# Optimization experiments

Hardware: AMD Instinct MI355X
Metric: run time of the kernel (lower is better)

Reference implementation:

```python
import jax, jax.numpy as jnp
import numpy as np

B, L, D = 4096, 50, 64
NU, NI, NR = 100000, 100000, 5


def setup_inputs() -> dict:
    key = jax.random.key(0)
    ks = jax.random.split(key, 16)
    s = 0.02
    inp = {
        "nodes_v": jax.random.randint(ks[0], (B,), 0, NI),
        "neigh_u": jax.random.randint(ks[1], (B, L), 0, NU),
        "neigh_r": jax.random.randint(ks[2], (B, L), 0, NR),
        "embed_u": jax.random.normal(ks[3], (NU, D)) * s,
        "embed_i": jax.random.normal(ks[4], (NI, D)) * s,
        "embed_r": jax.random.normal(ks[5], (NR, D)) * s,
        # gv MLP: Linear(2D,D) ReLU Linear(D,D) ReLU Linear(D,D)
        "gv_w1": jax.random.normal(ks[6], (2 * D, D)) * s, "gv_b1": jnp.zeros((D,)),
        "gv_w2": jax.random.normal(ks[7], (D, D)) * s,     "gv_b2": jnp.zeros((D,)),
        "gv_w3": jax.random.normal(ks[8], (D, D)) * s,     "gv_b3": jnp.zeros((D,)),
        # attention MLP: Linear(2D,D) ReLU Linear(D,D) ReLU Linear(D,1), softmax over neighbors
        "att_w1": jax.random.normal(ks[9], (2 * D, D)) * s, "att_b1": jnp.zeros((D,)),
        "att_w2": jax.random.normal(ks[10], (D, D)) * s,    "att_b2": jnp.zeros((D,)),
        "att_w3": jax.random.normal(ks[11], (D, 1)) * s,    "att_b3": jnp.zeros((1,)),
        # combine: Linear(2D,D) ReLU Linear(D,D) ReLU
        "wr1_w": jax.random.normal(ks[12], (2 * D, D)) * s, "wr1_b": jnp.zeros((D,)),
        "wr2_w": jax.random.normal(ks[13], (D, D)) * s,     "wr2_b": jnp.zeros((D,)),
    }
    return inp


def reference(nodes_v, neigh_u, neigh_r, embed_u, embed_i, embed_r,
              gv_w1, gv_b1, gv_w2, gv_b2, gv_w3, gv_b3,
              att_w1, att_b1, att_w2, att_b2, att_w3, att_b3,
              wr1_w, wr1_b, wr2_w, wr2_b):
    qj = embed_i[nodes_v]            # [B, D] item reps
    pt = embed_u[neigh_u]            # [B, L, D] neighbor user reps
    er = embed_r[neigh_r]            # [B, L, D] rating reps
    # fusion MLP g(.)
    x = jnp.concatenate([pt, er], axis=-1)                    # [B, L, 2D]
    h = jax.nn.relu(x @ gv_w1 + gv_b1)
    h = jax.nn.relu(h @ gv_w2 + gv_b2)
    fjt = h @ gv_w3 + gv_b3                                   # [B, L, D]
    # attention over neighbors (dropout is identity in eval mode)
    q_rep = jnp.broadcast_to(qj[:, None, :], fjt.shape)       # [B, L, D]
    a = jnp.concatenate([fjt, q_rep], axis=-1)                # [B, L, 2D]
    a = jax.nn.relu(a @ att_w1 + att_b1)
    a = jax.nn.relu(a @ att_w2 + att_b2)
    scores = (a @ att_w3 + att_b3)[..., 0]                    # [B, L]
    mu = jax.nn.softmax(scores, axis=1)                       # softmax over neighbors
    zj = jnp.einsum("bld,bl->bd", fjt, mu)                   # weighted aggregation
    # combine aggregated neighborhood with item's own embedding (2D -> D)
    z = jax.nn.relu(jnp.concatenate([zj, qj], axis=-1) @ wr1_w + wr1_b)
    out = jax.nn.relu(z @ wr2_w + wr2_b)                      # [B, D]
    return out
```

## Files before the change

kernel.cpp:

```cpp
#include <hip/hip_runtime.h>

typedef __bf16 bf16;
typedef short s16x8 __attribute__((ext_vector_type(8)));
typedef __bf16 b16x8 __attribute__((ext_vector_type(8)));
typedef float f32x4 __attribute__((ext_vector_type(4)));

#define B_   4096
#define L_   50
#define SH   72

#define OFF_W1F  0
#define OFF_W2F  8192
#define OFF_W3F  12288
#define OFF_WCF  16384
#define OFF_A2F  20480
#define OFF_R1T  24576
#define OFF_R2T  32768
#define WT_TOTAL 36864
#define BIAS1P_BYTE 73728
#define CQ_BYTE     73984
#define EU16_BYTE   1122560
#define ER16_BYTE   13922560
#define WS_NEED     13923200

#define PREP_W_BLOCKS 145
#define PREP_C_BLOCKS 1024
#define CONV_THREADS  800040
#define CONV_BLOCKS   3126

__device__ __forceinline__ unsigned short f2b(float f) {
    __bf16 h = (__bf16)f;
    return __builtin_bit_cast(unsigned short, h);
}
__device__ __forceinline__ unsigned pack2(float a, float b) {
    return (unsigned)f2b(a) | ((unsigned)f2b(b) << 16);
}
__device__ __forceinline__ s16x8 mkfrag(float4 a, float4 b) {
    union { s16x8 v; unsigned u[4]; } r;
    r.u[0] = pack2(a.x, a.y); r.u[1] = pack2(a.z, a.w);
    r.u[2] = pack2(b.x, b.y); r.u[3] = pack2(b.z, b.w);
    return r.v;
}
__device__ __forceinline__ f32x4 mfma16(s16x8 a, s16x8 b, f32x4 c) {
    return __builtin_amdgcn_mfma_f32_16x16x32_bf16(a, b, c, 0, 0, 0);
}

extern "C" __global__ void prep_all(const float* __restrict__ w1, const float* __restrict__ w2,
                                    const float* __restrict__ w3, const float* __restrict__ a1,
                                    const float* __restrict__ a2, const float* __restrict__ r1,
                                    const float* __restrict__ r2, const float* __restrict__ gb3,
                                    const float* __restrict__ ab1,
                                    const int* __restrict__ nodes_v, const float* __restrict__ embed_i,
                                    const float* __restrict__ embed_u, const float* __restrict__ embed_r,
                                    bf16* __restrict__ wt, float* __restrict__ bias1p,
                                    float* __restrict__ cq,
                                    bf16* __restrict__ eu16, bf16* __restrict__ er16)
{
    if (blockIdx.x >= PREP_W_BLOCKS + PREP_C_BLOCKS) {
        long t = (long)(blockIdx.x - PREP_W_BLOCKS - PREP_C_BLOCKS) * 256 + threadIdx.x;
        if (t < 800000) {
            const float* s = embed_u + t * 8;
            float4 a = *(const float4*)s, b = *(const float4*)(s + 4);
            *(s16x8*)(eu16 + t * 8) = mkfrag(a, b);
        } else if (t < CONV_THREADS) {
            long r = (t - 800000) * 8;
            const float* s = embed_r + r;
            float4 a = *(const float4*)s, b = *(const float4*)(s + 4);
            *(s16x8*)(er16 + r) = mkfrag(a, b);
        }
        return;
    }
    if (blockIdx.x >= PREP_W_BLOCKS) {
        int gid = (blockIdx.x - PREP_W_BLOCKS) * 256 + threadIdx.x;
        int b = gid >> 6, n = gid & 63;
        int v = nodes_v[b];
        const float* q = embed_i + v * 64;
        float s0 = 0.f, s1 = 0.f, s2 = 0.f, s3 = 0.f;
#pragma unroll
        for (int k = 0; k < 64; k += 4) {
            s0 = fmaf(q[k],     a1[(64 + k) * 64 + n],     s0);
            s1 = fmaf(q[k + 1], a1[(64 + k + 1) * 64 + n], s1);
            s2 = fmaf(q[k + 2], a1[(64 + k + 2) * 64 + n], s2);
            s3 = fmaf(q[k + 3], a1[(64 + k + 3) * 64 + n], s3);
        }
        cq[gid] = (s0 + s1) + (s2 + s3);
        return;
    }
    int i = blockIdx.x * 256 + threadIdx.x;
    if (i >= WT_TOTAL + 64) return;
    if (i >= WT_TOTAL) {
        int n = i - WT_TOTAL;
        float s0 = ab1[n], s1 = 0.f, s2 = 0.f, s3 = 0.f;
#pragma unroll
        for (int t = 0; t < 64; t += 4) {
            s0 = fmaf(gb3[t],     a1[t * 64 + n],       s0);
            s1 = fmaf(gb3[t + 1], a1[(t + 1) * 64 + n], s1);
            s2 = fmaf(gb3[t + 2], a1[(t + 2) * 64 + n], s2);
            s3 = fmaf(gb3[t + 3], a1[(t + 3) * 64 + n], s3);
        }
        bias1p[n] = (s0 + s1) + (s2 + s3);
        return;
    }
    float val;
    if (i < OFF_R1T) {
        int off, kind;
        if      (i < OFF_W2F) { off = OFF_W1F; kind = 0; }
        else if (i < OFF_W3F) { off = OFF_W2F; kind = 1; }
        else if (i < OFF_WCF) { off = OFF_W3F; kind = 2; }
        else if (i < OFF_A2F) { off = OFF_WCF; kind = 3; }
        else                  { off = OFF_A2F; kind = 4; }
        int local = i - off;
        int f = local >> 9, lane = (local >> 3) & 63, j = local & 7;
        int kt = f >> 2, nt = f & 3, quad = lane >> 4, m = lane & 15;
        int k = kt * 32 + quad * 8 + j;
        int n = nt * 16 + m;
        if (kind == 0)      val = w1[k * 64 + n];
        else if (kind == 1) val = w2[k * 64 + n];
        else if (kind == 2) val = w3[k * 64 + n];
        else if (kind == 4) val = a2[k * 64 + n];
        else {
            float s0 = 0.f, s1 = 0.f, s2 = 0.f, s3 = 0.f;
#pragma unroll
            for (int t = 0; t < 64; t += 4) {
                float4 w = *(const float4*)(w3 + k * 64 + t);
                s0 = fmaf(w.x, a1[t * 64 + n],       s0);
                s1 = fmaf(w.y, a1[(t + 1) * 64 + n], s1);
                s2 = fmaf(w.z, a1[(t + 2) * 64 + n], s2);
                s3 = fmaf(w.w, a1[(t + 3) * 64 + n], s3);
            }
            val = (s0 + s1) + (s2 + s3);
        }
    }
    else if (i < OFF_R2T) { int li = i - OFF_R1T; int n = li >> 7, k = li & 127; val = r1[k * 64 + n]; }
    else                  { int li = i - OFF_R2T; int n = li >> 6, k = li & 63;  val = r2[k * 64 + n]; }
    wt[i] = (bf16)val;
}

template<bool BF16E>
__global__ void __launch_bounds__(128, 4)
dense_fused(const int* __restrict__ nodes_v, const int* __restrict__ neigh_u,
            const int* __restrict__ neigh_r,
            const float* __restrict__ embed_u, const float* __restrict__ embed_i,
            const float* __restrict__ embed_r,
            const float* __restrict__ gv_b1, const float* __restrict__ gv_b2,
            const float* __restrict__ gv_b3,
            const float* __restrict__ att_b2, const float* __restrict__ att_w3,
            const float* __restrict__ wr1_b, const float* __restrict__ wr2_b,
            const bf16* __restrict__ wt, const bf16* __restrict__ eu16,
            const bf16* __restrict__ er16, const float* __restrict__ cq,
            const float* __restrict__ bias1p, float* __restrict__ out)
{
    __shared__ __align__(16) bf16 H[64 * SH];
    __shared__ float zp[2 * 64];
    __shared__ float swm[2 * 2];
    __shared__ float qsh[64];

    const int tid = threadIdx.x;
    const int lane = tid & 63, wave = tid >> 6;
    const int m = lane & 15, quad = lane >> 4;
    const int b = blockIdx.x;
    const int lbase = wave * 32;

    const int l0 = min(lbase + m, L_ - 1);
    const int l1 = min(lbase + 16 + m, L_ - 1);
    const int u0 = neigh_u[b * L_ + l0], u1 = neigh_u[b * L_ + l1];
    const int v0 = neigh_r[b * L_ + l0], v1 = neigh_r[b * L_ + l1];

    float cs4[4];
#pragma unroll
    for (int nt = 0; nt < 4; ++nt) {
        int c = nt * 16 + m;
        cs4[nt] = cq[b * 64 + c] + bias1p[c];
    }

    bf16* H0 = H + lbase * SH;
    bf16* H1 = H0 + 16 * SH;

    {
        f32x4 ac0[4] = {}, ac1[4] = {};
        if constexpr (BF16E) {
            const bf16* p00 = eu16 + (size_t)u0 * 64;
            const bf16* p01 = eu16 + (size_t)u1 * 64;
            const bf16* p10 = er16 + v0 * 64;
            const bf16* p11 = er16 + v1 * 64;
#pragma unroll
            for (int kt = 0; kt < 4; ++kt) {
                const bf16* s0p = (kt < 2 ? p00 : p10) + (kt & 1) * 32 + quad * 8;
                const bf16* s1p = (kt < 2 ? p01 : p11) + (kt & 1) * 32 + quad * 8;
                s16x8 a0 = *(const s16x8*)s0p;
                s16x8 a1 = *(const s16x8*)s1p;
#pragma unroll
                for (int nt = 0; nt < 4; ++nt) {
                    s16x8 bfr = *(const s16x8*)(wt + OFF_W1F + (kt * 4 + nt) * 512 + lane * 8);
                    ac0[nt] = mfma16(a0, bfr, ac0[nt]);
                    ac1[nt] = mfma16(a1, bfr, ac1[nt]);
                }
            }
        } else {
            const float* b00 = embed_u + (size_t)u0 * 64;
            const float* b01 = embed_u + (size_t)u1 * 64;
            const float* b10 = embed_r + v0 * 64;
            const float* b11 = embed_r + v1 * 64;
#pragma unroll
            for (int kt = 0; kt < 4; ++kt) {
                const float* s0p = (kt < 2 ? b00 : b10) + (kt & 1) * 32 + quad * 8;
                const float* s1p = (kt < 2 ? b01 : b11) + (kt & 1) * 32 + quad * 8;
                float4 a0a = *(const float4*)s0p, a0b = *(const float4*)(s0p + 4);
                float4 a1a = *(const float4*)s1p, a1b = *(const float4*)(s1p + 4);
                s16x8 a0 = mkfrag(a0a, a0b);
                s16x8 a1 = mkfrag(a1a, a1b);
#pragma unroll
                for (int nt = 0; nt < 4; ++nt) {
                    s16x8 bfr = *(const s16x8*)(wt + OFF_W1F + (kt * 4 + nt) * 512 + lane * 8);
                    ac0[nt] = mfma16(a0, bfr, ac0[nt]);
                    ac1[nt] = mfma16(a1, bfr, ac1[nt]);
                }
            }
        }
#pragma unroll
        for (int nt = 0; nt < 4; ++nt) {
            int c = nt * 16 + m;
            float bv = gv_b1[c];
#pragma unroll
            for (int r4 = 0; r4 < 4; ++r4) {
                H0[(quad * 4 + r4) * SH + c] = (bf16)fmaxf(ac0[nt][r4] + bv, 0.f);
                H1[(quad * 4 + r4) * SH + c] = (bf16)fmaxf(ac1[nt][r4] + bv, 0.f);
            }
        }
    }

    {
        f32x4 ac0[4] = {}, ac1[4] = {};
#pragma unroll
        for (int kt = 0; kt < 2; ++kt) {
            s16x8 a0 = *(const s16x8*)(H0 + m * SH + kt * 32 + quad * 8);
            s16x8 a1 = *(const s16x8*)(H1 + m * SH + kt * 32 + quad * 8);
#pragma unroll
            for (int nt = 0; nt < 4; ++nt) {
                s16x8 bfr = *(const s16x8*)(wt + OFF_W2F + (kt * 4 + nt) * 512 + lane * 8);
                ac0[nt] = mfma16(a0, bfr, ac0[nt]);
                ac1[nt] = mfma16(a1, bfr, ac1[nt]);
            }
        }
#pragma unroll
        for (int nt = 0; nt < 4; ++nt) {
            int c = nt * 16 + m;
            float bv = gv_b2[c];
#pragma unroll
            for (int r4 = 0; r4 < 4; ++r4) {
                H0[(quad * 4 + r4) * SH + c] = (bf16)fmaxf(ac0[nt][r4] + bv, 0.f);
                H1[(quad * 4 + r4) * SH + c] = (bf16)fmaxf(ac1[nt][r4] + bv, 0.f);
            }
        }
    }

    f32x4 aF0[4] = {}, aF1[4] = {};
    {
        f32x4 aA0[4] = {}, aA1[4] = {};
#pragma unroll
        for (int kt = 0; kt < 2; ++kt) {
            s16x8 a0 = *(const s16x8*)(H0 + m * SH + kt * 32 + quad * 8);
            s16x8 a1 = *(const s16x8*)(H1 + m * SH + kt * 32 + quad * 8);
#pragma unroll
            for (int nt = 0; nt < 4; ++nt) {
                s16x8 bF = *(const s16x8*)(wt + OFF_W3F + (kt * 4 + nt) * 512 + lane * 8);
                s16x8 bA = *(const s16x8*)(wt + OFF_WCF + (kt * 4 + nt) * 512 + lane * 8);
                aF0[nt] = mfma16(a0, bF, aF0[nt]);
                aF1[nt] = mfma16(a1, bF, aF1[nt]);
                aA0[nt] = mfma16(a0, bA, aA0[nt]);
                aA1[nt] = mfma16(a1, bA, aA1[nt]);
            }
        }
#pragma unroll
        for (int nt = 0; nt < 4; ++nt) {
            int c = nt * 16 + m;
#pragma unroll
            for (int r4 = 0; r4 < 4; ++r4) {
                H0[(quad * 4 + r4) * SH + c] = (bf16)fmaxf(aA0[nt][r4] + cs4[nt], 0.f);
                H1[(quad * 4 + r4) * SH + c] = (bf16)fmaxf(aA1[nt][r4] + cs4[nt], 0.f);
            }
        }
    }

    float s0[4], s1[4];
    {
        f32x4 ac0[4] = {}, ac1[4] = {};
#pragma unroll
        for (int kt = 0; kt < 2; ++kt) {
            s16x8 a0 = *(const s16x8*)(H0 + m * SH + kt * 32 + quad * 8);
            s16x8 a1 = *(const s16x8*)(H1 + m * SH + kt * 32 + quad * 8);
#pragma unroll
            for (int nt = 0; nt < 4; ++nt) {
                s16x8 bfr = *(const s16x8*)(wt + OFF_A2F + (kt * 4 + nt) * 512 + lane * 8);
                ac0[nt] = mfma16(a0, bfr, ac0[nt]);
                ac1[nt] = mfma16(a1, bfr, ac1[nt]);
            }
        }
#pragma unroll
        for (int r4 = 0; r4 < 4; ++r4) { s0[r4] = 0.f; s1[r4] = 0.f; }
#pragma unroll
        for (int nt = 0; nt < 4; ++nt) {
            int c = nt * 16 + m;
            float b2v = att_b2[c], w3v = att_w3[c];
#pragma unroll
            for (int r4 = 0; r4 < 4; ++r4) {
                s0[r4] += fmaxf(ac0[nt][r4] + b2v, 0.f) * w3v;
                s1[r4] += fmaxf(ac1[nt][r4] + b2v, 0.f) * w3v;
            }
        }
#pragma unroll
        for (int mask = 1; mask < 16; mask <<= 1)
#pragma unroll
            for (int r4 = 0; r4 < 4; ++r4) {
                s0[r4] += __shfl_xor(s0[r4], mask);
                s1[r4] += __shfl_xor(s1[r4], mask);
            }
    }

    {
        const int r0b = lbase + quad * 4;
        float mloc = -1e30f;
#pragma unroll
        for (int r4 = 0; r4 < 4; ++r4) {
            if (r0b + r4 < L_)      mloc = fmaxf(mloc, s0[r4]);
            if (r0b + 16 + r4 < L_) mloc = fmaxf(mloc, s1[r4]);
        }
        mloc = fmaxf(mloc, __shfl_xor(mloc, 16));
        mloc = fmaxf(mloc, __shfl_xor(mloc, 32));

        float e0[4], e1[4], ssum = 0.f;
#pragma unroll
        for (int r4 = 0; r4 < 4; ++r4) {
            e0[r4] = (r0b + r4 < L_)      ? __expf(s0[r4] - mloc) : 0.f;
            e1[r4] = (r0b + 16 + r4 < L_) ? __expf(s1[r4] - mloc) : 0.f;
            ssum += e0[r4] + e1[r4];
        }
        ssum += __shfl_xor(ssum, 16);
        ssum += __shfl_xor(ssum, 32);

        float z[4] = {0.f, 0.f, 0.f, 0.f};
#pragma unroll
        for (int r4 = 0; r4 < 4; ++r4)
#pragma unroll
            for (int nt = 0; nt < 4; ++nt)
                z[nt] += aF0[nt][r4] * e0[r4] + aF1[nt][r4] * e1[r4];
#pragma unroll
        for (int nt = 0; nt < 4; ++nt) {
            z[nt] += __shfl_xor(z[nt], 16);
            z[nt] += __shfl_xor(z[nt], 32);
        }
        if (quad == 0) {
#pragma unroll
            for (int nt = 0; nt < 4; ++nt) zp[wave * 64 + nt * 16 + m] = z[nt];
        }
        if (lane == 0) { swm[wave * 2] = ssum; swm[wave * 2 + 1] = mloc; }
    }
    __syncthreads();

    if (wave == 0) {
        const int d = lane;
        float ma = swm[1], mb = swm[3];
        float sa = swm[0], sb = swm[2];
        float M  = fmaxf(ma, mb);
        float fa = __expf(ma - M), fb = __expf(mb - M);
        float zj = (fa * zp[d] + fb * zp[64 + d]) / (fa * sa + fb * sb) + gv_b3[d];

        float* zsh = zp;
        zsh[d] = zj;
        qsh[d] = embed_i[nodes_v[b] * 64 + d];

        float accz = wr1_b[d];
        const bf16* r1 = wt + OFF_R1T + d * 128;
#pragma unroll
        for (int k8 = 0; k8 < 8; ++k8) {
            b16x8 wv = *(const b16x8*)(r1 + k8 * 8);
#pragma unroll
            for (int j = 0; j < 8; ++j) accz = fmaf((float)wv[j], zsh[k8 * 8 + j], accz);
        }
#pragma unroll
        for (int k8 = 0; k8 < 8; ++k8) {
            b16x8 wv = *(const b16x8*)(r1 + 64 + k8 * 8);
#pragma unroll
            for (int j = 0; j < 8; ++j) accz = fmaf((float)wv[j], qsh[k8 * 8 + j], accz);
        }
        zsh[d] = fmaxf(accz, 0.f);

        float acco = wr2_b[d];
        const bf16* r2 = wt + OFF_R2T + d * 64;
#pragma unroll
        for (int k8 = 0; k8 < 8; ++k8) {
            b16x8 wv = *(const b16x8*)(r2 + k8 * 8);
#pragma unroll
            for (int j = 0; j < 8; ++j) acco = fmaf((float)wv[j], zsh[k8 * 8 + j], acco);
        }
        out[b * 64 + d] = fmaxf(acco, 0.f);
    }
}

extern "C" void kernel_launch(void* const* d_in, const int* in_sizes, int n_in,
                              void* d_out, int out_size, void* d_ws, size_t ws_size,
                              hipStream_t stream)
{
    const int* nodes_v = (const int*)d_in[0];
    const int* neigh_u = (const int*)d_in[1];
    const int* neigh_r = (const int*)d_in[2];
    const float* embed_u = (const float*)d_in[3];
    const float* embed_i = (const float*)d_in[4];
    const float* embed_r = (const float*)d_in[5];
    const float* gv_w1  = (const float*)d_in[6];  const float* gv_b1 = (const float*)d_in[7];
    const float* gv_w2  = (const float*)d_in[8];  const float* gv_b2 = (const float*)d_in[9];
    const float* gv_w3  = (const float*)d_in[10]; const float* gv_b3 = (const float*)d_in[11];
    const float* att_w1 = (const float*)d_in[12]; const float* att_b1 = (const float*)d_in[13];
    const float* att_w2 = (const float*)d_in[14]; const float* att_b2 = (const float*)d_in[15];
    const float* att_w3 = (const float*)d_in[16]; const float* att_b3 = (const float*)d_in[17];
    const float* wr1_w  = (const float*)d_in[18]; const float* wr1_b = (const float*)d_in[19];
    const float* wr2_w  = (const float*)d_in[20]; const float* wr2_b = (const float*)d_in[21];
    (void)att_b3;

    bf16*  wt     = (bf16*)d_ws;
    float* bias1p = (float*)((char*)d_ws + BIAS1P_BYTE);
    float* cq     = (float*)((char*)d_ws + CQ_BYTE);
    bf16*  eu16   = (bf16*)((char*)d_ws + EU16_BYTE);
    bf16*  er16   = (bf16*)((char*)d_ws + ER16_BYTE);

    const bool big = ws_size >= (size_t)WS_NEED;
    const int prep_grid = PREP_W_BLOCKS + PREP_C_BLOCKS + (big ? CONV_BLOCKS : 0);

    prep_all<<<prep_grid, 256, 0, stream>>>(
        gv_w1, gv_w2, gv_w3, att_w1, att_w2, wr1_w, wr2_w, gv_b3, att_b1,
        nodes_v, embed_i, embed_u, embed_r, wt, bias1p, cq, eu16, er16);

    if (big) {
        dense_fused<true><<<B_, 128, 0, stream>>>(nodes_v, neigh_u, neigh_r,
                                                  embed_u, embed_i, embed_r,
                                                  gv_b1, gv_b2, gv_b3, att_b2, att_w3,
                                                  wr1_b, wr2_b, wt, eu16, er16,
                                                  cq, bias1p, (float*)d_out);
    } else {
        dense_fused<false><<<B_, 128, 0, stream>>>(nodes_v, neigh_u, neigh_r,
                                                   embed_u, embed_i, embed_r,
                                                   gv_b1, gv_b2, gv_b3, att_b2, att_w3,
                                                   wr1_b, wr2_b, wt, eu16, er16,
                                                   cq, bias1p, (float*)d_out);
    }
}
```

Measured before the change: 164.6 us.

## Compute item-query projection with MFMA and process two items per block

The cq prep step, which projects each item embedding through the second half of att_w1, now runs on bf16 MFMA tiles over 32 blocks instead of a scalar FMA loop over 1024 blocks. The fused dense kernel now handles two batch items per 256-thread block (four waves) instead of one item per 128-thread block, with the shared buffers doubled and the softmax-merge and combine epilogue indexed per item. This cuts prep work and block count. The cost is bf16 rounding in cq and a lower launch-bounds occupancy hint.

```diff
diff --git a/kernel.cpp b/kernel.cpp
--- a/kernel.cpp
+++ b/kernel.cpp
@@ -24,7 +24,7 @@
 #define WS_NEED     13923200
 
 #define PREP_W_BLOCKS 145
-#define PREP_C_BLOCKS 1024
+#define CQ_BLOCKS     32
 #define CONV_THREADS  800040
 #define CONV_BLOCKS   3126
 
@@ -56,8 +56,8 @@
                                     float* __restrict__ cq,
                                     bf16* __restrict__ eu16, bf16* __restrict__ er16)
 {
-    if (blockIdx.x >= PREP_W_BLOCKS + PREP_C_BLOCKS) {
-        long t = (long)(blockIdx.x - PREP_W_BLOCKS - PREP_C_BLOCKS) * 256 + threadIdx.x;
+    if (blockIdx.x >= PREP_W_BLOCKS + CQ_BLOCKS) {
+        long t = (long)(blockIdx.x - PREP_W_BLOCKS - CQ_BLOCKS) * 256 + threadIdx.x;
         if (t < 800000) {
             const float* s = embed_u + t * 8;
             float4 a = *(const float4*)s, b = *(const float4*)(s + 4);
@@ -71,19 +71,47 @@
         return;
     }
     if (blockIdx.x >= PREP_W_BLOCKS) {
-        int gid = (blockIdx.x - PREP_W_BLOCKS) * 256 + threadIdx.x;
-        int b = gid >> 6, n = gid & 63;
-        int v = nodes_v[b];
-        const float* q = embed_i + v * 64;
-        float s0 = 0.f, s1 = 0.f, s2 = 0.f, s3 = 0.f;
-#pragma unroll
-        for (int k = 0; k < 64; k += 4) {
-            s0 = fmaf(q[k],     a1[(64 + k) * 64 + n],     s0);
-            s1 = fmaf(q[k + 1], a1[(64 + k + 1) * 64 + n], s1);
-            s2 = fmaf(q[k + 2], a1[(64 + k + 2) * 64 + n], s2);
-            s3 = fmaf(q[k + 3], a1[(64 + k + 3) * 64 + n], s3);
-        }
-        cq[gid] = (s0 + s1) + (s2 + s3);
+        int wv   = (blockIdx.x - PREP_W_BLOCKS) * 4 + (threadIdx.x >> 6);
+        int lane = threadIdx.x & 63, m = lane & 15, quad = lane >> 4;
+        int base = wv * 32;
+        int i0 = base + m, i1 = base + 16 + m;
+        int v0 = nodes_v[i0], v1 = nodes_v[i1];
+
+        s16x8 bfr[8];
+#pragma unroll
+        for (int kt = 0; kt < 2; ++kt)
+#pragma unroll
+            for (int nt = 0; nt < 4; ++nt) {
+                const float* src = a1 + (64 + kt * 32 + quad * 8) * 64 + nt * 16 + m;
+                union { s16x8 v; unsigned u[4]; } fr;
+#pragma unroll
+                for (int jj = 0; jj < 4; ++jj)
+                    fr.u[jj] = pack2(src[(2 * jj) * 64], src[(2 * jj + 1) * 64]);
+                bfr[kt * 4 + nt] = fr.v;
+            }
+
+        f32x4 ac0[4] = {}, ac1[4] = {};
+#pragma unroll
+        for (int kt = 0; kt < 2; ++kt) {
+            const float* q0 = embed_i + (size_t)v0 * 64 + kt * 32 + quad * 8;
+            const float* q1 = embed_i + (size_t)v1 * 64 + kt * 32 + quad * 8;
+            s16x8 aq0 = mkfrag(*(const float4*)q0, *(const float4*)(q0 + 4));
+            s16x8 aq1 = mkfrag(*(const float4*)q1, *(const float4*)(q1 + 4));
+#pragma unroll
+            for (int nt = 0; nt < 4; ++nt) {
+                ac0[nt] = mfma16(aq0, bfr[kt * 4 + nt], ac0[nt]);
+                ac1[nt] = mfma16(aq1, bfr[kt * 4 + nt], ac1[nt]);
+            }
+        }
+#pragma unroll
+        for (int nt = 0; nt < 4; ++nt) {
+            int c = nt * 16 + m;
+#pragma unroll
+            for (int r4 = 0; r4 < 4; ++r4) {
+                cq[(base + quad * 4 + r4) * 64 + c]      = ac0[nt][r4];
+                cq[(base + 16 + quad * 4 + r4) * 64 + c] = ac1[nt][r4];
+            }
+        }
         return;
     }
     int i = blockIdx.x * 256 + threadIdx.x;
@@ -137,7 +165,7 @@
 }
 
 template<bool BF16E>
-__global__ void __launch_bounds__(128, 4)
+__global__ void __launch_bounds__(256, 2)
 dense_fused(const int* __restrict__ nodes_v, const int* __restrict__ neigh_u,
             const int* __restrict__ neigh_r,
             const float* __restrict__ embed_u, const float* __restrict__ embed_i,
@@ -150,31 +178,35 @@
             const bf16* __restrict__ er16, const float* __restrict__ cq,
             const float* __restrict__ bias1p, float* __restrict__ out)
 {
-    __shared__ __align__(16) bf16 H[64 * SH];
-    __shared__ float zp[2 * 64];
-    __shared__ float swm[2 * 2];
-    __shared__ float qsh[64];
+    __shared__ __align__(16) bf16 H[128 * SH];
+    __shared__ float zp[4 * 64];
+    __shared__ float swm[4 * 2];
+    __shared__ float qsh[2 * 64];
 
     const int tid = threadIdx.x;
     const int lane = tid & 63, wave = tid >> 6;
     const int m = lane & 15, quad = lane >> 4;
-    const int b = blockIdx.x;
-    const int lbase = wave * 32;
-
+    const int b0 = blockIdx.x * 2;
+    const int rw0 = wave * 32;
+    const int item_w = rw0 >> 6;
+    const int lbase = rw0 & 63;
+
+    const int bw = b0 + item_w;
     const int l0 = min(lbase + m, L_ - 1);
     const int l1 = min(lbase + 16 + m, L_ - 1);
-    const int u0 = neigh_u[b * L_ + l0], u1 = neigh_u[b * L_ + l1];
-    const int v0 = neigh_r[b * L_ + l0], v1 = neigh_r[b * L_ + l1];
+    const int u0 = neigh_u[bw * L_ + l0], u1 = neigh_u[bw * L_ + l1];
+    const int v0 = neigh_r[bw * L_ + l0], v1 = neigh_r[bw * L_ + l1];
 
     float cs4[4];
 #pragma unroll
     for (int nt = 0; nt < 4; ++nt) {
         int c = nt * 16 + m;
-        cs4[nt] = cq[b * 64 + c] + bias1p[c];
-    }
-
-    bf16* H0 = H + lbase * SH;
-    bf16* H1 = H0 + 16 * SH;
+        cs4[nt] = cq[bw * 64 + c] + bias1p[c];
+    }
+
+    bf16* Hw = H + rw0 * SH;
+    bf16* H0 = Hw;
+    bf16* H1 = Hw + 16 * SH;
 
     {
         f32x4 ac0[4] = {}, ac1[4] = {};
@@ -357,17 +389,19 @@
     }
     __syncthreads();
 
-    if (wave == 0) {
+    if ((wave & 1) == 0) {
+        const int item = wave >> 1;
         const int d = lane;
-        float ma = swm[1], mb = swm[3];
-        float sa = swm[0], sb = swm[2];
+        float ma = swm[wave * 2 + 1],      mb = swm[(wave + 1) * 2 + 1];
+        float sa = swm[wave * 2],          sb = swm[(wave + 1) * 2];
         float M  = fmaxf(ma, mb);
         float fa = __expf(ma - M), fb = __expf(mb - M);
-        float zj = (fa * zp[d] + fb * zp[64 + d]) / (fa * sa + fb * sb) + gv_b3[d];
-
-        float* zsh = zp;
+        float zj = (fa * zp[wave * 64 + d] + fb * zp[(wave + 1) * 64 + d])
+                 / (fa * sa + fb * sb) + gv_b3[d];
+
+        float* zsh = zp + wave * 64;
         zsh[d] = zj;
-        qsh[d] = embed_i[nodes_v[b] * 64 + d];
+        qsh[item * 64 + d] = embed_i[nodes_v[b0 + item] * 64 + d];
 
         float accz = wr1_b[d];
         const bf16* r1 = wt + OFF_R1T + d * 128;
@@ -381,7 +415,7 @@
         for (int k8 = 0; k8 < 8; ++k8) {
             b16x8 wv = *(const b16x8*)(r1 + 64 + k8 * 8);
 #pragma unroll
-            for (int j = 0; j < 8; ++j) accz = fmaf((float)wv[j], qsh[k8 * 8 + j], accz);
+            for (int j = 0; j < 8; ++j) accz = fmaf((float)wv[j], qsh[item * 64 + k8 * 8 + j], accz);
         }
         zsh[d] = fmaxf(accz, 0.f);
 
@@ -393,7 +427,7 @@
 #pragma unroll
             for (int j = 0; j < 8; ++j) acco = fmaf((float)wv[j], zsh[k8 * 8 + j], acco);
         }
-        out[b * 64 + d] = fmaxf(acco, 0.f);
+        out[(b0 + item) * 64 + d] = fmaxf(acco, 0.f);
     }
 }
 
@@ -424,23 +458,23 @@
     bf16*  er16   = (bf16*)((char*)d_ws + ER16_BYTE);
 
     const bool big = ws_size >= (size_t)WS_NEED;
-    const int prep_grid = PREP_W_BLOCKS + PREP_C_BLOCKS + (big ? CONV_BLOCKS : 0);
+    const int prep_grid = PREP_W_BLOCKS + CQ_BLOCKS + (big ? CONV_BLOCKS : 0);
 
     prep_all<<<prep_grid, 256, 0, stream>>>(
         gv_w1, gv_w2, gv_w3, att_w1, att_w2, wr1_w, wr2_w, gv_b3, att_b1,
         nodes_v, embed_i, embed_u, embed_r, wt, bias1p, cq, eu16, er16);
 
     if (big) {
-        dense_fused<true><<<B_, 128, 0, stream>>>(nodes_v, neigh_u, neigh_r,
-                                                  embed_u, embed_i, embed_r,
-                                                  gv_b1, gv_b2, gv_b3, att_b2, att_w3,
-                                                  wr1_b, wr2_b, wt, eu16, er16,
-                                                  cq, bias1p, (float*)d_out);
+        dense_fused<true><<<B_ / 2, 256, 0, stream>>>(nodes_v, neigh_u, neigh_r,
+                                                      embed_u, embed_i, embed_r,
+                                                      gv_b1, gv_b2, gv_b3, att_b2, att_w3,
+                                                      wr1_b, wr2_b, wt, eu16, er16,
+                                                      cq, bias1p, (float*)d_out);
     } else {
-        dense_fused<false><<<B_, 128, 0, stream>>>(nodes_v, neigh_u, neigh_r,
-                                                   embed_u, embed_i, embed_r,
-                                                   gv_b1, gv_b2, gv_b3, att_b2, att_w3,
-                                                   wr1_b, wr2_b, wt, eu16, er16,
-                                                   cq, bias1p, (float*)d_out);
-    }
-}
+        dense_fused<false><<<B_ / 2, 256, 0, stream>>>(nodes_v, neigh_u, neigh_r,
+                                                       embed_u, embed_i, embed_r,
+                                                       gv_b1, gv_b2, gv_b3, att_b2, att_w3,
+                                                       wr1_b, wr2_b, wt, eu16, er16,
+                                                       cq, bias1p, (float*)d_out);
+    }
+}
```

Result: faster. 159.3 us (median of 2 runs) (-3.2%).
